# Kernel optimization log

Hardware: AMD Instinct MI355X
Metric: run time of the kernel (lower is better)

Reference implementation:

```python
import jax, jax.numpy as jnp
import numpy as np

B, T, D, H, DFF, E = 4, 1024, 1024, 16, 4096, 8
DH = D // H
EPS = 1e-6


def setup_inputs() -> dict:
    key = jax.random.key(0)
    ks = jax.random.split(key, 16)
    s = 0.02
    return {
        "x": jax.random.normal(ks[0], (B, T, D), jnp.float32),
        "mask": jnp.ones((B, 1, 1, T), jnp.bool_),
        "Wq": jax.random.normal(ks[1], (D, D), jnp.float32) * s,
        "bq": jnp.zeros((D,), jnp.float32),
        "Wk": jax.random.normal(ks[2], (D, D), jnp.float32) * s,
        "bk": jnp.zeros((D,), jnp.float32),
        "Wv": jax.random.normal(ks[3], (D, D), jnp.float32) * s,
        "bv": jnp.zeros((D,), jnp.float32),
        "Wo": jax.random.normal(ks[4], (D, D), jnp.float32) * s,
        "bo": jnp.zeros((D,), jnp.float32),
        "ln1_a": jnp.ones((D,), jnp.float32),
        "ln1_b": jnp.zeros((D,), jnp.float32),
        "ln2_a": jnp.ones((D,), jnp.float32),
        "ln2_b": jnp.zeros((D,), jnp.float32),
        "gW": jax.random.normal(ks[5], (D, E), jnp.float32) * s,
        "gb": jnp.zeros((E,), jnp.float32),
        "W1": jax.random.normal(ks[6], (E, D, DFF), jnp.float32) * s,
        "b1": jnp.zeros((E, DFF), jnp.float32),
        "W2": jax.random.normal(ks[7], (E, DFF, D), jnp.float32) * s,
        "b2": jnp.zeros((E, D), jnp.float32),
    }


def layer_norm(x, a, b):
    # Faithful to source: torch std is unbiased (ddof=1), divides by (std + eps)
    mean = jnp.mean(x, -1, keepdims=True)
    std = jnp.std(x, -1, keepdims=True, ddof=1)
    return a * (x - mean) / (std + EPS) + b


def mha(x, mask, Wq, bq, Wk, bk, Wv, bv, Wo, bo):
    def split(h):
        return h.reshape(B, T, H, DH).transpose(0, 2, 1, 3)  # [B,H,T,DH]
    q = split(x @ Wq + bq)
    k = split(x @ Wk + bk)
    v = split(x @ Wv + bv)
    scores = jnp.einsum("bhqd,bhkd->bhqk", q, k) / jnp.sqrt(jnp.float32(DH))
    scores = jnp.where(mask, scores, jnp.float32(-1e9))
    attn = jax.nn.softmax(scores, axis=-1)
    out = jnp.einsum("bhqk,bhkd->bhqd", attn, v)
    out = out.transpose(0, 2, 1, 3).reshape(B, T, D)
    return out @ Wo + bo


def moe(xf, gW, gb, W1, b1, W2, b2):
    # xf: [N, D] flat tokens; top-1 Switch routing
    gate_probs = jax.nn.softmax(xf @ gW + gb, axis=-1)  # [N, E]
    top1_idx = jnp.argmax(gate_probs, axis=-1)          # [N]
    top1_p = jnp.max(gate_probs, axis=-1)               # [N]
    out = jnp.zeros_like(xf)
    for e in range(E):  # fixed small structural loop over experts
        h = jax.nn.relu(xf @ W1[e] + b1[e])
        oe = h @ W2[e] + b2[e]
        sel = (top1_idx == e).astype(xf.dtype)
        out = out + (sel * top1_p)[:, None] * oe
    counts = jax.nn.one_hot(top1_idx, E, dtype=jnp.float32).sum(0)
    aux_loss = jnp.sum((counts / (B * T)) ** 2) * E
    return out, aux_loss


def reference(x, mask, Wq, bq, Wk, bk, Wv, bv, Wo, bo,
              ln1_a, ln1_b, ln2_a, ln2_b, gW, gb, W1, b1, W2, b2):
    # sublayer[0]: x + attn(norm(x))  (dropout=0, inference)
    x1 = x + mha(layer_norm(x, ln1_a, ln1_b), mask, Wq, bq, Wk, bk, Wv, bv, Wo, bo)
    # MoE applied to x1 directly (source calls feed_forward(x), not on the norm)
    ff_out, aux_loss = moe(x1.reshape(-1, D), gW, gb, W1, b1, W2, b2)
    # sublayer[1] with lambda _: ff_out  -> x1 + ff_out (norm computed but discarded)
    x2 = x1 + ff_out.reshape(B, T, D)
    return x2, aux_loss
```

## Files before the change

kernel.cpp:

```cpp
#include <hip/hip_runtime.h>

#define DEV __device__ __forceinline__

typedef unsigned short u16;
typedef __bf16 bf16x8 __attribute__((ext_vector_type(8)));
typedef float f32x4 __attribute__((ext_vector_type(4)));

static constexpr int Bn = 4, Tn = 1024, Dn = 1024, Hn = 16, DFFn = 4096, En = 8;
static constexpr int Nn = Bn * Tn;
static constexpr int MAXT2 = 24;
static constexpr int MAXT1 = 40;
static constexpr int HROWS = 6144;

static constexpr int MT2_E = 0, MT2_P0 = 24;
static constexpr int MT1_E = 48, MT1_P0 = 88;
static constexpr int MCNT = 128, MCUR = 136, MSEG = 144, MPERM = 152;

static constexpr size_t WQKVT_O = 0;
static constexpr size_t WOT_O   = WQKVT_O + 3ull * 1024 * 1024 * 2;
static constexpr size_t W12T_O  = WOT_O + 1ull * 1024 * 1024 * 2;
static constexpr size_t X1F_O   = W12T_O + 8ull * 1024 * 4096 * 2;
static constexpr size_t XN_O    = X1F_O + (size_t)Nn * Dn * 4;
static constexpr size_t Q_O     = XN_O + (size_t)Nn * Dn * 2;
static constexpr size_t K_O     = Q_O + (size_t)Nn * Dn * 2;
static constexpr size_t VT_O    = K_O + (size_t)Nn * Dn * 2;
static constexpr size_t X1B_O   = VT_O + (size_t)Nn * Dn * 2;
static constexpr size_t P3_O    = XN_O;
static constexpr size_t H_O     = X1B_O + (size_t)Nn * Dn * 2;
static constexpr size_t TOPP_O  = H_O + (size_t)HROWS * DFFn * 2;
static constexpr size_t TIDX_O  = TOPP_O + (size_t)Nn * 4;
static constexpr size_t META_O  = TIDX_O + (size_t)Nn * 4;

DEV u16 f2bf(float f) {
  union { float f; unsigned u; } v; v.f = f;
  unsigned r = v.u + 0x7fffu + ((v.u >> 16) & 1u);
  return (u16)(r >> 16);
}
DEV float bf2f(u16 x) {
  union { unsigned u; float f; } v; v.u = ((unsigned)x) << 16;
  return v.f;
}

DEV void gload16(const void* g, void* l) {
  __builtin_amdgcn_global_load_lds(
      (__attribute__((address_space(1))) void*)(void*)g,
      (__attribute__((address_space(3))) void*)l, 16, 0, 0);
}

template <int N> DEV void waitvm() {
  if constexpr (N == 0) asm volatile("s_waitcnt vmcnt(0)" ::: "memory");
  else if constexpr (N == 8) asm volatile("s_waitcnt vmcnt(8)" ::: "memory");
}

DEV void sdecode64(int o, int& row, int& c) {
  row = o >> 7;
  c = ((o >> 4) & 7) ^ (row & 7);
}

DEV int aswz(int r, int c) { return c ^ (r & 7) ^ (((r >> 3) & 3) << 1); }

__global__ __launch_bounds__(256) void tcast_kernel(
    const float* __restrict__ src, u16* __restrict__ dst,
    int R, int C, long srcBatch, long dstBatch) {
  __shared__ u16 tile[64][65];
  src += (long)blockIdx.z * srcBatch;
  dst += (long)blockIdx.z * dstBatch;
  int r0 = blockIdx.y * 64, c0 = blockIdx.x * 64;
  int tr = threadIdx.x >> 4;
  int tc = (threadIdx.x & 15) * 4;
#pragma unroll
  for (int i = 0; i < 4; i++) {
    int r = tr + i * 16;
    float4 v = *reinterpret_cast<const float4*>(&src[(long)(r0 + r) * C + c0 + tc]);
    tile[r][tc + 0] = f2bf(v.x); tile[r][tc + 1] = f2bf(v.y);
    tile[r][tc + 2] = f2bf(v.z); tile[r][tc + 3] = f2bf(v.w);
  }
  __syncthreads();
#pragma unroll
  for (int i = 0; i < 4; i++) {
    int r = tr + i * 16;
    ushort4 o;
    o.x = tile[tc + 0][r]; o.y = tile[tc + 1][r];
    o.z = tile[tc + 2][r]; o.w = tile[tc + 3][r];
    *reinterpret_cast<ushort4*>(&dst[(long)(c0 + r) * R + r0 + tc]) = o;
  }
}

__global__ __launch_bounds__(256) void ln_kernel(
    const float* __restrict__ x, const float* __restrict__ a,
    const float* __restrict__ b, u16* __restrict__ xn) {
  __shared__ float red[8];
  int row = blockIdx.x, tid = threadIdx.x;
  int lane = tid & 63, w = tid >> 6;
  float4 v = *reinterpret_cast<const float4*>(&x[(size_t)row * 1024 + tid * 4]);
  float s = v.x + v.y + v.z + v.w;
  float sq = v.x * v.x + v.y * v.y + v.z * v.z + v.w * v.w;
#pragma unroll
  for (int sh = 1; sh <= 32; sh <<= 1) { s += __shfl_xor(s, sh); sq += __shfl_xor(sq, sh); }
  if (lane == 0) { red[w] = s; red[4 + w] = sq; }
  __syncthreads();
  s = red[0] + red[1] + red[2] + red[3];
  sq = red[4] + red[5] + red[6] + red[7];
  float mean = s * (1.0f / 1024.0f);
  float var = (sq - s * mean) * (1.0f / 1023.0f);
  float inv = 1.0f / (sqrtf(var) + 1e-6f);
  float4 av = *reinterpret_cast<const float4*>(&a[tid * 4]);
  float4 bv = *reinterpret_cast<const float4*>(&b[tid * 4]);
  ushort4 o;
  o.x = f2bf(av.x * (v.x - mean) * inv + bv.x);
  o.y = f2bf(av.y * (v.y - mean) * inv + bv.y);
  o.z = f2bf(av.z * (v.z - mean) * inv + bv.z);
  o.w = f2bf(av.w * (v.w - mean) * inv + bv.w);
  *reinterpret_cast<ushort4*>(&xn[(size_t)row * 1024 + tid * 4]) = o;
}

template <int MODE, int NG>
__global__ __launch_bounds__(512, 2) void gemm8_k(
    const u16* __restrict__ Ag, const u16* __restrict__ Bg,
    const float* __restrict__ f0, const float* __restrict__ f1,
    const float* __restrict__ f2, u16* __restrict__ ob0, u16* __restrict__ ob1,
    u16* __restrict__ ob2, const int* __restrict__ meta) {
  constexpr int NSUB = 16;
  constexpr int MT = (MODE == 0) ? 16 : MAXT2;
  constexpr int NT = (MODE == 0) ? 12 : 16;

  __shared__ u16 As[2][256 * 64];
  __shared__ u16 Bs[2][256 * 64];

  const int tid = threadIdx.x, lane = tid & 63, w = tid >> 6;
  const int wm = w >> 2, wn = w & 3;
  const int cL = lane >> 4, rl15 = lane & 15;

  constexpr int NWG = MT * NT;
  constexpr int q8 = NWG >> 3;
  int b = blockIdx.x;
  int lg = (b & 7) * q8 + (b >> 3);
  constexpr int PERG = MT * NG;
  int g = lg / PERG, rem = lg - g * PERG;
  int mt = rem / NG;
  int nt = g * NG + (rem - (rem / NG) * NG);

  int m0 = mt * 256, n0 = nt * 256;
  const u16* Bbase = Bg;
  int e = 0, cnt = 0, seg = 0, pos0 = 0;
  if constexpr (MODE == 2) {
    e = meta[MT2_E + mt];
    if (e < 0) return;
    cnt = meta[MCNT + e];
    seg = meta[MSEG + e];
    pos0 = meta[MT2_P0 + mt];
    Bbase = Bg + (size_t)e * 4096 * 1024;
  }

  const u16* gA[4];
  const u16* gB[4];
#pragma unroll
  for (int j = 0; j < 4; j++) {
    int row, c;
    sdecode64(j * 8192 + tid * 16, row, c);
    if constexpr (MODE == 2) {
      int pos = pos0 + row; if (pos >= cnt) pos = cnt - 1;
      int tok = meta[MPERM + seg + pos];
      gA[j] = Ag + (size_t)tok * 1024 + c * 8;
    } else {
      gA[j] = Ag + (size_t)(m0 + row) * 1024 + c * 8;
    }
    gB[j] = Bbase + (size_t)(n0 + row) * 1024 + c * 8;
  }

  auto STAGE = [&](int t) {
    int bi = t & 1;
#pragma unroll
    for (int j = 0; j < 4; j++)
      gload16(gA[j] + t * 64, &As[bi][j * 4096 + tid * 8]);
#pragma unroll
    for (int j = 0; j < 4; j++)
      gload16(gB[j] + t * 64, &Bs[bi][j * 4096 + tid * 8]);
  };

  f32x4 acc[8][4] = {};

  STAGE(0);
  STAGE(1);
  waitvm<8>();
  __builtin_amdgcn_s_barrier();

  for (int t = 0;; t++) {
    const char* Ab = reinterpret_cast<const char*>(&As[t & 1][0]);
    const char* Bb = reinterpret_cast<const char*>(&Bs[t & 1][0]);
#pragma unroll
    for (int kh = 0; kh < 2; kh++) {
      bf16x8 bfr[4];
#pragma unroll
      for (int ni = 0; ni < 4; ni++) {
        int row = wn * 64 + ni * 16 + rl15;
        bfr[ni] = *reinterpret_cast<const bf16x8*>(
            Bb + row * 128 + ((kh * 64 + cL * 16) ^ ((row & 7) << 4)));
      }
#pragma unroll
      for (int h = 0; h < 2; h++) {
        bf16x8 af[4];
#pragma unroll
        for (int mi2 = 0; mi2 < 4; mi2++) {
          int row = wm * 128 + h * 64 + mi2 * 16 + rl15;
          af[mi2] = *reinterpret_cast<const bf16x8*>(
              Ab + row * 128 + ((kh * 64 + cL * 16) ^ ((row & 7) << 4)));
        }
        __builtin_amdgcn_s_setprio(1);
#pragma unroll
        for (int mi2 = 0; mi2 < 4; mi2++)
#pragma unroll
          for (int ni = 0; ni < 4; ni++)
            acc[h * 4 + mi2][ni] = __builtin_amdgcn_mfma_f32_16x16x32_bf16(
                af[mi2], bfr[ni], acc[h * 4 + mi2][ni], 0, 0, 0);
        __builtin_amdgcn_s_setprio(0);
      }
    }
    if (t == NSUB - 1) break;
    asm volatile("s_waitcnt lgkmcnt(0)" ::: "memory");
    __builtin_amdgcn_sched_barrier(0);
    __builtin_amdgcn_s_barrier();
    if (t + 2 < NSUB) { STAGE(t + 2); waitvm<8>(); }
    else waitvm<0>();
    __builtin_amdgcn_s_barrier();
  }

  const int cl = rl15, rl = cL;
  if constexpr (MODE == 0) {
    int third = n0 >> 10;
    const float* bias = (third == 0) ? f0 : (third == 1) ? f1 : f2;
    const float qs = (third == 0) ? 0.125f : 1.0f;
#pragma unroll
    for (int ni = 0; ni < 4; ni++) {
      int col = n0 + wn * 64 + ni * 16 + cl;
      int jj = col & 1023;
      float bb_ = bias[jj];
      int hh = jj >> 6, dd = jj & 63;
#pragma unroll
      for (int mi = 0; mi < 8; mi++) {
        int t0 = m0 + wm * 128 + mi * 16 + rl * 4;
        int b_ = t0 >> 10, tt = t0 & 1023;
        size_t bh = (size_t)(b_ * Hn + hh);
        if (third == 2) {
          ushort4 o4;
          o4.x = f2bf(acc[mi][ni][0] + bb_); o4.y = f2bf(acc[mi][ni][1] + bb_);
          o4.z = f2bf(acc[mi][ni][2] + bb_); o4.w = f2bf(acc[mi][ni][3] + bb_);
          *reinterpret_cast<ushort4*>(&ob2[(bh * 64 + dd) * 1024 + tt]) = o4;
        } else {
          u16* dst = (third == 0) ? ob0 : ob1;
#pragma unroll
          for (int r = 0; r < 4; r++)
            dst[(bh * 1024 + tt + r) * 64 + dd] = f2bf((acc[mi][ni][r] + bb_) * qs);
        }
      }
    }
  } else {
#pragma unroll
    for (int ni = 0; ni < 4; ni++) {
      int col = n0 + wn * 64 + ni * 16 + cl;
      float b1_ = f0[(size_t)e * 4096 + col];
#pragma unroll
      for (int mi = 0; mi < 8; mi++) {
        int pos = pos0 + wm * 128 + mi * 16 + rl * 4;
#pragma unroll
        for (int r = 0; r < 4; r++) {
          float v = acc[mi][ni][r] + b1_;
          v = v > 0.0f ? v : 0.0f;
          ob0[(size_t)(seg + pos + r) * 4096 + col] = f2bf(v);
        }
      }
    }
  }
}

template <int MODE, int BM, int NG, int KSPLIT>
__global__ __launch_bounds__(256, 3) void gemm3_k(
    const u16* __restrict__ Ag, const u16* __restrict__ Bg,
    const float* __restrict__ f0, const float* __restrict__ xres,
    float* __restrict__ x1f, u16* __restrict__ ob0,
    u16* __restrict__ pout, const int* __restrict__ meta) {
  constexpr int K = (MODE == 3) ? 4096 : 1024;
  constexpr int KS = K / KSPLIT;
  constexpr int NSUB = KS >> 6;
  constexpr int MT = (MODE == 1) ? (4096 / BM) : MAXT1;
  constexpr int NT = 8;
  constexpr int WR = BM / 2;
  constexpr int MI = WR / 16;
  constexpr int CA = BM / 32;

  __shared__ u16 As[BM * 64];
  __shared__ u16 Bs[128 * 64];

  const int tid = threadIdx.x, lane = tid & 63, w = tid >> 6;
  const int wm = w >> 1, wn = w & 1;
  const int cL = lane >> 4, rl15 = lane & 15;

  constexpr int NWG = MT * NT * KSPLIT;
  constexpr int q8 = NWG >> 3;
  int b = blockIdx.x;
  int lg = (b & 7) * q8 + (b >> 3);
  constexpr int PERG = KSPLIT * MT * NG;
  int g = lg / PERG, rem = lg - g * PERG;
  int s = rem / (MT * NG); rem -= s * (MT * NG);
  int mt = rem / NG;
  int nt = g * NG + (rem - (rem / NG) * NG);

  int m0 = mt * BM, n0 = nt * 128;
  const int k0 = s * KS;
  const u16* Abase = Ag;
  const u16* Bbase = Bg;
  int e = 0, seg = 0, pos0 = 0;
  if constexpr (MODE == 3) {
    e = meta[MT1_E + mt];
    if (e < 0) return;
    seg = meta[MSEG + e];
    pos0 = meta[MT1_P0 + mt];
    Bbase = Bg + (size_t)e * 4096 * 1024;
    Abase = Ag + (size_t)(seg + pos0) * 4096;
    m0 = 0;
  }

  const u16* gA[CA];
  const u16* gB[4];
#pragma unroll
  for (int j = 0; j < CA; j++) {
    int row, c;
    sdecode64(j * 4096 + tid * 16, row, c);
    gA[j] = Abase + (size_t)(m0 + row) * K + k0 + c * 8;
  }
#pragma unroll
  for (int j = 0; j < 4; j++) {
    int row, c;
    sdecode64(j * 4096 + tid * 16, row, c);
    gB[j] = Bbase + (size_t)(n0 + row) * K + k0 + c * 8;
  }

  auto STAGE = [&](int t) {
#pragma unroll
    for (int j = 0; j < CA; j++)
      gload16(gA[j] + t * 64, &As[j * 2048 + tid * 8]);
#pragma unroll
    for (int j = 0; j < 4; j++)
      gload16(gB[j] + t * 64, &Bs[j * 2048 + tid * 8]);
  };

  f32x4 acc[MI][4] = {};
  const char* Ab = reinterpret_cast<const char*>(&As[0]);
  const char* Bb = reinterpret_cast<const char*>(&Bs[0]);

  STAGE(0);
  for (int t = 0; t < NSUB; t++) {
    asm volatile("s_waitcnt vmcnt(0)" ::: "memory");
    __builtin_amdgcn_s_barrier();
#pragma unroll
    for (int ph = 0; ph < 2; ph++) {
      bf16x8 af[MI], bfr[4];
#pragma unroll
      for (int mi = 0; mi < MI; mi++) {
        int row = wm * WR + mi * 16 + rl15;
        af[mi] = *reinterpret_cast<const bf16x8*>(
            Ab + row * 128 + ((ph * 64 + cL * 16) ^ ((row & 7) << 4)));
      }
#pragma unroll
      for (int ni = 0; ni < 4; ni++) {
        int row = wn * 64 + ni * 16 + rl15;
        bfr[ni] = *reinterpret_cast<const bf16x8*>(
            Bb + row * 128 + ((ph * 64 + cL * 16) ^ ((row & 7) << 4)));
      }
#pragma unroll
      for (int mi = 0; mi < MI; mi++)
#pragma unroll
        for (int ni = 0; ni < 4; ni++)
          acc[mi][ni] = __builtin_amdgcn_mfma_f32_16x16x32_bf16(
              af[mi], bfr[ni], acc[mi][ni], 0, 0, 0);
    }
    __builtin_amdgcn_s_barrier();
    if (t + 1 < NSUB) STAGE(t + 1);
  }

  const int cl = rl15, rl = cL;
  if constexpr (MODE == 1) {
#pragma unroll
    for (int ni = 0; ni < 4; ni++) {
      int col = n0 + wn * 64 + ni * 16 + cl;
      float bo_ = f0[col];
#pragma unroll
      for (int mi = 0; mi < MI; mi++) {
        int row = m0 + wm * WR + mi * 16 + rl * 4;
#pragma unroll
        for (int r = 0; r < 4; r++) {
          size_t idx = (size_t)(row + r) * 1024 + col;
          float v = acc[mi][ni][r] + bo_ + xres[idx];
          x1f[idx] = v;
          ob0[idx] = f2bf(v);
        }
      }
    }
  } else {
#pragma unroll
    for (int ni = 0; ni < 4; ni++) {
      int col = n0 + wn * 64 + ni * 16 + cl;
#pragma unroll
      for (int mi = 0; mi < MI; mi++) {
        int pos = pos0 + wm * WR + mi * 16 + rl * 4;
#pragma unroll
        for (int r = 0; r < 4; r++)
          pout[((size_t)s * HROWS + seg + pos + r) * 1024 + col] = f2bf(acc[mi][ni][r]);
      }
    }
  }
}

__global__ __launch_bounds__(256) void reduce3_kernel(
    const u16* __restrict__ P3, const float* __restrict__ x1f,
    const float* __restrict__ topp, const float* __restrict__ b2,
    const int* __restrict__ meta, float* __restrict__ out) {
  int bidx = blockIdx.x;
  int tile = bidx >> 7, rowin = bidx & 127;
  int e = meta[MT1_E + tile];
  if (e < 0) return;
  int cnt = meta[MCNT + e], seg = meta[MSEG + e];
  int pos = meta[MT1_P0 + tile] + rowin;
  if (pos >= cnt) return;
  int tok = meta[MPERM + seg + pos];
  size_t prow = (size_t)(seg + pos) * 1024;
  float p = topp[tok];
  int c = threadIdx.x * 4;
  ushort4 u0 = *reinterpret_cast<const ushort4*>(&P3[prow + c]);
  ushort4 u1 = *reinterpret_cast<const ushort4*>(&P3[(size_t)HROWS * 1024 + prow + c]);
  float4 xr = *reinterpret_cast<const float4*>(&x1f[(size_t)tok * 1024 + c]);
  float4 bb = *reinterpret_cast<const float4*>(&b2[e * 1024 + c]);
  float4 o;
  o.x = xr.x + p * (bf2f(u0.x) + bf2f(u1.x) + bb.x);
  o.y = xr.y + p * (bf2f(u0.y) + bf2f(u1.y) + bb.y);
  o.z = xr.z + p * (bf2f(u0.z) + bf2f(u1.z) + bb.z);
  o.w = xr.w + p * (bf2f(u0.w) + bf2f(u1.w) + bb.w);
  *reinterpret_cast<float4*>(&out[(size_t)tok * 1024 + c]) = o;
}

__global__ __launch_bounds__(256, 4) void attn_kernel(
    const u16* __restrict__ q, const u16* __restrict__ k,
    const u16* __restrict__ vt, u16* __restrict__ attn) {
  __shared__ u16 Ks[2][64 * 64];
  __shared__ u16 Vs[2][64 * 64];
  const int tid = threadIdx.x, lane = tid & 63, w = tid >> 6;
  const int g = lane >> 4, l15 = lane & 15;

  int bb = blockIdx.x;
  int lg = (bb & 7) * 128 + (bb >> 3);
  const int bh = lg >> 4;
  const int qt = lg & 15;
  const size_t qkbase = (size_t)bh * Tn * 64;
  const size_t vtbase = (size_t)bh * 64 * Tn;
  const int qrow0 = qt * 64 + w * 16;

  bf16x8 qf[2];
  {
    const u16* qp = q + qkbase + (size_t)(qrow0 + l15) * 64 + g * 8;
    qf[0] = *reinterpret_cast<const bf16x8*>(qp);
    qf[1] = *reinterpret_cast<const bf16x8*>(qp + 32);
  }

  const u16* gk[2];
  const u16* gv[2];
#pragma unroll
  for (int j = 0; j < 2; j++) {
    int sidx = j * 256 + tid;
    int r = sidx >> 3, p = sidx & 7;
    int c = aswz(r, p);
    gk[j] = k + qkbase + (size_t)r * 64 + c * 8;
    gv[j] = vt + vtbase + (size_t)r * Tn + c * 8;
  }

  auto STAGE = [&](int t) {
    int buf = t & 1;
#pragma unroll
    for (int j = 0; j < 2; j++) {
      int sidx = j * 256 + tid;
      gload16(gk[j] + (size_t)t * 4096, &Ks[buf][sidx * 8]);
      gload16(gv[j] + (size_t)t * 64, &Vs[buf][sidx * 8]);
    }
  };

  f32x4 o[4] = {};
  float mrun = -1e30f, lsum = 0.0f;

  STAGE(0);
  for (int t = 0; t < 16; t++) {
    asm volatile("s_waitcnt vmcnt(0)" ::: "memory");
    __builtin_amdgcn_s_barrier();
    if (t + 1 < 16) STAGE(t + 1);

    const char* Kb = reinterpret_cast<const char*>(&Ks[t & 1][0]);
    const char* Vb = reinterpret_cast<const char*>(&Vs[t & 1][0]);

    f32x4 sk[2][2];
#pragma unroll
    for (int kb = 0; kb < 2; kb++)
#pragma unroll
      for (int m = 0; m < 2; m++) {
        f32x4 sa = {};
#pragma unroll
        for (int ph = 0; ph < 2; ph++) {
          int ksel = kb * 32 + (l15 >> 2) * 8 + m * 4 + (lane & 3);
          int pch = aswz(ksel, g + ph * 4);
          bf16x8 kf = *reinterpret_cast<const bf16x8*>(Kb + ksel * 128 + pch * 16);
          sa = __builtin_amdgcn_mfma_f32_16x16x32_bf16(kf, qf[ph], sa, 0, 0, 0);
        }
        sk[kb][m] = sa;
      }

    float mx = -1e30f;
#pragma unroll
    for (int kb = 0; kb < 2; kb++)
#pragma unroll
      for (int m = 0; m < 2; m++)
#pragma unroll
        for (int r = 0; r < 4; r++) mx = fmaxf(mx, sk[kb][m][r]);
    mx = fmaxf(mx, __shfl_xor(mx, 16));
    mx = fmaxf(mx, __shfl_xor(mx, 32));
    float mn = fmaxf(mrun, mx);
    float rsc = __expf(mrun - mn);
    mrun = mn;

    float pv[2][8];
    float ps = 0.0f;
#pragma unroll
    for (int kb = 0; kb < 2; kb++)
#pragma unroll
      for (int m = 0; m < 2; m++)
#pragma unroll
        for (int r = 0; r < 4; r++) {
          float pe = __expf(sk[kb][m][r] - mn);
          pv[kb][m * 4 + r] = pe;
          ps += pe;
        }
    ps += __shfl_xor(ps, 16);
    ps += __shfl_xor(ps, 32);
    lsum = lsum * rsc + ps;
#pragma unroll
    for (int nf = 0; nf < 4; nf++)
#pragma unroll
      for (int r = 0; r < 4; r++) o[nf][r] *= rsc;

    bf16x8 pf[2];
#pragma unroll
    for (int kb = 0; kb < 2; kb++)
#pragma unroll
      for (int j = 0; j < 8; j++) pf[kb][j] = (__bf16)pv[kb][j];

#pragma unroll
    for (int nf = 0; nf < 4; nf++) {
      int d = nf * 16 + l15;
#pragma unroll
      for (int kb = 0; kb < 2; kb++) {
        int pch = aswz(d, g + kb * 4);
        bf16x8 vf = *reinterpret_cast<const bf16x8*>(Vb + d * 128 + pch * 16);
        o[nf] = __builtin_amdgcn_mfma_f32_16x16x32_bf16(vf, pf[kb], o[nf], 0, 0, 0);
      }
    }
  }

  float inv = 1.0f / lsum;
  int b_ = bh >> 4, h_ = bh & 15;
  int tok = qrow0 + l15;
#pragma unroll
  for (int nf = 0; nf < 4; nf++)
#pragma unroll
    for (int r = 0; r < 4; r++) {
      int d = nf * 16 + g * 4 + r;
      attn[((size_t)(b_ * Tn + tok)) * 1024 + h_ * 64 + d] = f2bf(o[nf][r] * inv);
    }
}

__global__ __launch_bounds__(256) void gate_kernel(
    const float* __restrict__ x1f, const float* __restrict__ gW,
    const float* __restrict__ gb, float* __restrict__ topp,
    int* __restrict__ tidx, int* __restrict__ meta) {
  int lane = threadIdx.x & 63;
  int n = blockIdx.x * 4 + (threadIdx.x >> 6);
  float acc[8] = {};
  const float* xr = x1f + (size_t)n * 1024;
  for (int kk = 0; kk < 16; kk++) {
    int kcol = kk * 64 + lane;
    float xv = xr[kcol];
    float4 g0 = *reinterpret_cast<const float4*>(&gW[kcol * 8]);
    float4 g1 = *reinterpret_cast<const float4*>(&gW[kcol * 8 + 4]);
    acc[0] = fmaf(xv, g0.x, acc[0]); acc[1] = fmaf(xv, g0.y, acc[1]);
    acc[2] = fmaf(xv, g0.z, acc[2]); acc[3] = fmaf(xv, g0.w, acc[3]);
    acc[4] = fmaf(xv, g1.x, acc[4]); acc[5] = fmaf(xv, g1.y, acc[5]);
    acc[6] = fmaf(xv, g1.z, acc[6]); acc[7] = fmaf(xv, g1.w, acc[7]);
  }
#pragma unroll
  for (int e2 = 0; e2 < 8; e2++)
#pragma unroll
    for (int sh = 1; sh <= 32; sh <<= 1) acc[e2] += __shfl_xor(acc[e2], sh);
  if (lane == 0) {
    float best = -1e30f; int bi = 0;
#pragma unroll
    for (int e2 = 0; e2 < 8; e2++) {
      float lgt = acc[e2] + gb[e2];
      if (lgt > best) { best = lgt; bi = e2; }
    }
    float den = 0.0f;
#pragma unroll
    for (int e2 = 0; e2 < 8; e2++) den += __expf(acc[e2] + gb[e2] - best);
    topp[n] = 1.0f / den;
    tidx[n] = bi;
    atomicAdd(&meta[MCNT + bi], 1);
  }
}

__global__ void scan_kernel(int* meta, float* aux_out) {
  if (threadIdx.x == 0) {
    int sb = 0, t2 = 0, t1 = 0;
    float aux = 0.0f;
    for (int e2 = 0; e2 < 8; e2++) {
      meta[MSEG + e2] = sb;
      int c = meta[MCNT + e2];
      int n2 = (c + 255) >> 8;
      for (int i = 0; i < n2; i++) { meta[MT2_E + t2] = e2; meta[MT2_P0 + t2] = i * 256; t2++; }
      int n1 = (c + 127) >> 7;
      for (int i = 0; i < n1; i++) { meta[MT1_E + t1] = e2; meta[MT1_P0 + t1] = i * 128; t1++; }
      sb += n2 << 8;
      float fr = (float)c * (1.0f / 4096.0f);
      aux += fr * fr;
    }
    for (; t2 < MAXT2; t2++) { meta[MT2_E + t2] = -1; meta[MT2_P0 + t2] = 0; }
    for (; t1 < MAXT1; t1++) { meta[MT1_E + t1] = -1; meta[MT1_P0 + t1] = 0; }
    aux_out[0] = aux * 8.0f;
  }
}

__global__ __launch_bounds__(256) void scatter_kernel(const int* __restrict__ tidx, int* meta) {
  int n = blockIdx.x * 256 + threadIdx.x;
  int e2 = tidx[n];
  int pos = atomicAdd(&meta[MCUR + e2], 1);
  meta[MPERM + meta[MSEG + e2] + pos] = n;
}

extern "C" void kernel_launch(void* const* d_in, const int* in_sizes, int n_in,
                              void* d_out, int out_size, void* d_ws, size_t ws_size,
                              hipStream_t stream) {
  const float* x   = (const float*)d_in[0];
  const float* Wq  = (const float*)d_in[2];
  const float* bq  = (const float*)d_in[3];
  const float* Wk  = (const float*)d_in[4];
  const float* bk  = (const float*)d_in[5];
  const float* Wv  = (const float*)d_in[6];
  const float* bv  = (const float*)d_in[7];
  const float* Wo  = (const float*)d_in[8];
  const float* bo  = (const float*)d_in[9];
  const float* ln1a = (const float*)d_in[10];
  const float* ln1b = (const float*)d_in[11];
  const float* gW  = (const float*)d_in[14];
  const float* gb  = (const float*)d_in[15];
  const float* W1  = (const float*)d_in[16];
  const float* b1  = (const float*)d_in[17];
  const float* W2  = (const float*)d_in[18];
  const float* b2  = (const float*)d_in[19];
  float* out = (float*)d_out;
  char* ws = (char*)d_ws;

  u16* wqkvt = (u16*)(ws + WQKVT_O);
  u16* wot   = (u16*)(ws + WOT_O);
  u16* w12t  = (u16*)(ws + W12T_O);
  u16* xn    = (u16*)(ws + XN_O);
  u16* qb    = (u16*)(ws + Q_O);
  u16* kb    = (u16*)(ws + K_O);
  u16* vtb   = (u16*)(ws + VT_O);
  float* x1f = (float*)(ws + X1F_O);
  u16* x1b   = (u16*)(ws + X1B_O);
  u16* p3    = (u16*)(ws + P3_O);
  u16* hb    = (u16*)(ws + H_O);
  float* topp = (float*)(ws + TOPP_O);
  int* tidx  = (int*)(ws + TIDX_O);
  int* meta  = (int*)(ws + META_O);

  hipMemsetAsync(meta + MCNT, 0, 16 * sizeof(int), stream);

  tcast_kernel<<<dim3(16, 16, 1), 256, 0, stream>>>(Wq, wqkvt, 1024, 1024, 0, 0);
  tcast_kernel<<<dim3(16, 16, 1), 256, 0, stream>>>(Wk, wqkvt + 1024 * 1024, 1024, 1024, 0, 0);
  tcast_kernel<<<dim3(16, 16, 1), 256, 0, stream>>>(Wv, wqkvt + 2 * 1024 * 1024, 1024, 1024, 0, 0);
  tcast_kernel<<<dim3(16, 16, 1), 256, 0, stream>>>(Wo, wot, 1024, 1024, 0, 0);
  tcast_kernel<<<dim3(64, 16, 8), 256, 0, stream>>>(W1, w12t, 1024, 4096,
                                                    (long)1024 * 4096, (long)4096 * 1024);

  ln_kernel<<<4096, 256, 0, stream>>>(x, ln1a, ln1b, xn);
  gemm8_k<0, 4><<<192, 512, 0, stream>>>(xn, wqkvt, bq, bk, bv, qb, kb, vtb, meta);
  attn_kernel<<<1024, 256, 0, stream>>>(qb, kb, vtb, xn);
  gemm3_k<1, 64, 4, 1><<<512, 256, 0, stream>>>(xn, wot, bo, x, x1f, x1b, nullptr, meta);
  gate_kernel<<<1024, 256, 0, stream>>>(x1f, gW, gb, topp, tidx, meta);
  scan_kernel<<<1, 64, 0, stream>>>(meta, out + (size_t)Nn * Dn);
  scatter_kernel<<<16, 256, 0, stream>>>(tidx, meta);
  gemm8_k<2, 4><<<384, 512, 0, stream>>>(x1b, w12t, b1, nullptr, nullptr, hb, nullptr,
                                         nullptr, meta);
  tcast_kernel<<<dim3(16, 64, 8), 256, 0, stream>>>(W2, w12t, 4096, 1024,
                                                    (long)4096 * 1024, (long)1024 * 4096);
  gemm3_k<3, 128, 2, 2><<<640, 256, 0, stream>>>(hb, w12t, nullptr, nullptr, nullptr,
                                                 nullptr, p3, meta);
  reduce3_kernel<<<MAXT1 * 128, 256, 0, stream>>>(p3, x1f, topp, b2, meta, out);
}
```

Baseline: 422.1 us.

## Interleave LDS fragment reads, MFMA blocks and split global prefetch in GEMM loop

Restructures the GEMM main loop into four quarter-tile MFMA phases. Each phase is preceded by targeted LDS fragment reads with partial lgkmcnt waits, so math can start before all fragments arrive. The next tile's global-to-LDS loads are split into four slots spread across the phases, which leaves only one barrier pair per iteration. In exchange, A fragments are re-read from LDS once per iteration and more fragment registers are live at once, which adds LDS traffic and register pressure.

```diff
diff --git a/kernel.cpp b/kernel.cpp
--- a/kernel.cpp
+++ b/kernel.cpp
@@ -47,17 +47,14 @@
       (__attribute__((address_space(3))) void*)l, 16, 0, 0);
 }
 
-template <int N> DEV void waitvm() {
-  if constexpr (N == 0) asm volatile("s_waitcnt vmcnt(0)" ::: "memory");
-  else if constexpr (N == 8) asm volatile("s_waitcnt vmcnt(8)" ::: "memory");
-}
-
 DEV void sdecode64(int o, int& row, int& c) {
   row = o >> 7;
   c = ((o >> 4) & 7) ^ (row & 7);
 }
 
 DEV int aswz(int r, int c) { return c ^ (r & 7) ^ (((r >> 3) & 3) << 1); }
+
+#define SBAR __builtin_amdgcn_sched_barrier(0)
 
 __global__ __launch_bounds__(256) void tcast_kernel(
     const float* __restrict__ src, u16* __restrict__ dst,
@@ -114,6 +111,40 @@
   *reinterpret_cast<ushort4*>(&xn[(size_t)row * 1024 + tid * 4]) = o;
 }
 
+#define RD_A8(dst, Abase_, q)                                               \
+  _Pragma("unroll")                                                         \
+  for (int mi = 0; mi < 4; mi++)                                            \
+    _Pragma("unroll")                                                       \
+    for (int kk = 0; kk < 2; kk++) {                                        \
+      int row_ = wm * 128 + (q) * 64 + mi * 16 + rl15;                      \
+      dst[mi * 2 + kk] = *reinterpret_cast<const bf16x8*>(                  \
+          Abase_ + row_ * 128 + ((kk * 64 + cL * 16) ^ ((row_ & 7) << 4))); \
+    }
+
+#define RD_B4(dst, Bbase_, q)                                               \
+  _Pragma("unroll")                                                         \
+  for (int ni = 0; ni < 2; ni++)                                            \
+    _Pragma("unroll")                                                       \
+    for (int kk = 0; kk < 2; kk++) {                                        \
+      int row_ = wn * 64 + (q) * 32 + ni * 16 + rl15;                       \
+      dst[ni * 2 + kk] = *reinterpret_cast<const bf16x8*>(                  \
+          Bbase_ + row_ * 128 + ((kk * 64 + cL * 16) ^ ((row_ & 7) << 4))); \
+    }
+
+#define MM16(Aq, Bq, asrc, bsrc)                                            \
+  __builtin_amdgcn_s_setprio(1);                                            \
+  _Pragma("unroll")                                                         \
+  for (int mi = 0; mi < 4; mi++)                                            \
+    _Pragma("unroll")                                                       \
+    for (int ni = 0; ni < 2; ni++)                                          \
+      _Pragma("unroll")                                                     \
+      for (int kk = 0; kk < 2; kk++)                                        \
+        acc[(Aq) * 4 + mi][(Bq) * 2 + ni] =                                 \
+            __builtin_amdgcn_mfma_f32_16x16x32_bf16(                        \
+                asrc[mi * 2 + kk], bsrc[ni * 2 + kk],                       \
+                acc[(Aq) * 4 + mi][(Bq) * 2 + ni], 0, 0, 0);                \
+  __builtin_amdgcn_s_setprio(0);
+
 template <int MODE, int NG>
 __global__ __launch_bounds__(512, 2) void gemm8_k(
     const u16* __restrict__ Ag, const u16* __restrict__ Bg,
@@ -168,61 +199,66 @@
     gB[j] = Bbase + (size_t)(n0 + row) * 1024 + c * 8;
   }
 
-  auto STAGE = [&](int t) {
-    int bi = t & 1;
-#pragma unroll
-    for (int j = 0; j < 4; j++)
-      gload16(gA[j] + t * 64, &As[bi][j * 4096 + tid * 8]);
-#pragma unroll
-    for (int j = 0; j < 4; j++)
-      gload16(gB[j] + t * 64, &Bs[bi][j * 4096 + tid * 8]);
-  };
+#define STAGE_SLOT(t, slot)                                                   \
+  {                                                                           \
+    int bi_ = (t) & 1;                                                        \
+    if constexpr ((slot) == 0) {                                              \
+      gload16(gA[0] + (t) * 64, &As[bi_][0 * 4096 + tid * 8]);                \
+      gload16(gA[1] + (t) * 64, &As[bi_][1 * 4096 + tid * 8]);                \
+    } else if constexpr ((slot) == 1) {                                       \
+      gload16(gB[0] + (t) * 64, &Bs[bi_][0 * 4096 + tid * 8]);                \
+      gload16(gB[1] + (t) * 64, &Bs[bi_][1 * 4096 + tid * 8]);                \
+    } else if constexpr ((slot) == 2) {                                       \
+      gload16(gA[2] + (t) * 64, &As[bi_][2 * 4096 + tid * 8]);                \
+      gload16(gA[3] + (t) * 64, &As[bi_][3 * 4096 + tid * 8]);                \
+    } else {                                                                  \
+      gload16(gB[2] + (t) * 64, &Bs[bi_][2 * 4096 + tid * 8]);                \
+      gload16(gB[3] + (t) * 64, &Bs[bi_][3 * 4096 + tid * 8]);                \
+    }                                                                         \
+  }
 
   f32x4 acc[8][4] = {};
-
-  STAGE(0);
-  STAGE(1);
-  waitvm<8>();
+  bf16x8 a0[8], a1[8], b0[4], b1[4];
+
+  STAGE_SLOT(0, 0) STAGE_SLOT(0, 1) STAGE_SLOT(0, 2) STAGE_SLOT(0, 3)
+  STAGE_SLOT(1, 0)
+  asm volatile("s_waitcnt vmcnt(2)" ::: "memory");
   __builtin_amdgcn_s_barrier();
 
-  for (int t = 0;; t++) {
+  for (int t = 0; t < NSUB; t++) {
     const char* Ab = reinterpret_cast<const char*>(&As[t & 1][0]);
     const char* Bb = reinterpret_cast<const char*>(&Bs[t & 1][0]);
-#pragma unroll
-    for (int kh = 0; kh < 2; kh++) {
-      bf16x8 bfr[4];
-#pragma unroll
-      for (int ni = 0; ni < 4; ni++) {
-        int row = wn * 64 + ni * 16 + rl15;
-        bfr[ni] = *reinterpret_cast<const bf16x8*>(
-            Bb + row * 128 + ((kh * 64 + cL * 16) ^ ((row & 7) << 4)));
-      }
-#pragma unroll
-      for (int h = 0; h < 2; h++) {
-        bf16x8 af[4];
-#pragma unroll
-        for (int mi2 = 0; mi2 < 4; mi2++) {
-          int row = wm * 128 + h * 64 + mi2 * 16 + rl15;
-          af[mi2] = *reinterpret_cast<const bf16x8*>(
-              Ab + row * 128 + ((kh * 64 + cL * 16) ^ ((row & 7) << 4)));
-        }
-        __builtin_amdgcn_s_setprio(1);
-#pragma unroll
-        for (int mi2 = 0; mi2 < 4; mi2++)
-#pragma unroll
-          for (int ni = 0; ni < 4; ni++)
-            acc[h * 4 + mi2][ni] = __builtin_amdgcn_mfma_f32_16x16x32_bf16(
-                af[mi2], bfr[ni], acc[h * 4 + mi2][ni], 0, 0, 0);
-        __builtin_amdgcn_s_setprio(0);
-      }
-    }
-    if (t == NSUB - 1) break;
-    asm volatile("s_waitcnt lgkmcnt(0)" ::: "memory");
-    __builtin_amdgcn_sched_barrier(0);
-    __builtin_amdgcn_s_barrier();
-    if (t + 2 < NSUB) { STAGE(t + 2); waitvm<8>(); }
-    else waitvm<0>();
-    __builtin_amdgcn_s_barrier();
+
+    RD_A8(a0, Ab, 0)
+    RD_B4(b0, Bb, 0)
+    RD_A8(a1, Ab, 1)
+    if (t + 1 < NSUB) STAGE_SLOT(t + 1, 1)
+    SBAR; asm volatile("s_waitcnt lgkmcnt(8)" ::: "memory"); SBAR;
+    MM16(0, 0, a0, b0)
+
+    RD_B4(b1, Bb, 1)
+    if (t + 1 < NSUB) STAGE_SLOT(t + 1, 2)
+    SBAR; asm volatile("s_waitcnt lgkmcnt(4)" ::: "memory"); SBAR;
+    MM16(1, 0, a1, b0)
+
+    RD_A8(a0, Ab, 0)
+    if (t + 1 < NSUB) STAGE_SLOT(t + 1, 3)
+    SBAR; asm volatile("s_waitcnt lgkmcnt(8)" ::: "memory"); SBAR;
+    MM16(1, 1, a1, b1)
+
+    SBAR; asm volatile("s_waitcnt lgkmcnt(0)" ::: "memory"); SBAR;
+    MM16(0, 1, a0, b1)
+
+    if (t + 1 < NSUB) {
+      __builtin_amdgcn_s_barrier();
+      if (t + 2 < NSUB) {
+        STAGE_SLOT(t + 2, 0)
+        asm volatile("s_waitcnt vmcnt(2)" ::: "memory");
+      } else {
+        asm volatile("s_waitcnt vmcnt(0)" ::: "memory");
+      }
+      __builtin_amdgcn_s_barrier();
+    }
   }
 
   const int cl = rl15, rl = cL;
```

Measured after the change: 415.7 us. Within noise of the previous version (-1.5%).
